# Optimization experiments

Hardware: AMD Instinct MI355X
Metric: run time of the kernel (lower is better)

Reference implementation:

```python
import jax, jax.numpy as jnp
import numpy as np


def setup_inputs() -> dict:
    key = jax.random.key(0)
    k1, k2, k3, k4, k5 = jax.random.split(key, 5)
    b, c, l, h, w = 16, 64, 8, 56, 56
    cl = c * l
    return {
        "inpt": jax.random.normal(k1, (b, c, l, h, w), dtype=jnp.float32),
        "theta_w": jax.random.normal(k2, (cl,), dtype=jnp.float32) * (1.0 / np.sqrt(cl)),
        "g_w": jax.random.normal(k3, (cl,), dtype=jnp.float32) * (1.0 / np.sqrt(cl)),
        "h_w": jax.random.normal(k4, (cl,), dtype=jnp.float32),
        "h_b": jax.random.normal(k5, (cl,), dtype=jnp.float32) * 0.1,
    }


def reference(inpt, theta_w, g_w, h_w, h_b):
    # inpt: [b, c, l, h, w] -> flatten channel/time to cl and space to n = h*w
    b, c, l, h, w = inpt.shape
    cl, n = c * l, h * w
    x = inpt.reshape(b, cl, n)  # [b, cl, n]

    # 1x1 convs (bias=False) projecting cl -> 1 channel
    t = jnp.einsum("bcn,c->bn", x, theta_w)  # theta(inpt): [b, n]
    g = jnp.einsum("bcn,c->bn", x, g_w)      # g(inpt):     [b, n]

    # torch: outer product t (b,1,n) * g^T (b,n,1) -> [b,n,n], AvgPool1d(n) over last dim
    # mathematically: att[b,i] = g[b,i] * mean_j t[b,j]
    att = g * jnp.mean(t, axis=1, keepdims=True)  # [b, n]

    # h: 1x1 conv 1 -> cl channels with bias, then residual add
    out = x + att[:, None, :] * h_w[None, :, None] + h_b[None, :, None]  # [b, cl, n]
    return out.reshape(b, cl, h, w)
```

## Files before the change

kernel.cpp:

```cpp
#include <hip/hip_runtime.h>

#define BATCH 16
#define CL    512
#define NSP   3136
#define N4    (NSP / 4)
#define CGROUPS 4
#define CPG   (CL / CGROUPS)

__global__ __launch_bounds__(256) void sa_pass1(
    const float* __restrict__ x,
    const float* __restrict__ theta_w,
    const float* __restrict__ g_w,
    float* __restrict__ g_out,
    float* __restrict__ m_out)
{
    const int b     = blockIdx.x;
    const int chunk = blockIdx.y;
    const int tid   = threadIdx.x;
    const int tx    = tid & 63;
    const int ty    = tid >> 6;
    const int i4    = chunk * 64 + tx;
    const bool valid = (i4 < N4);

    const float4* xb = (const float4*)(x + (size_t)b * CL * NSP);

    float4 gv = make_float4(0.f, 0.f, 0.f, 0.f);
    float4 tv = make_float4(0.f, 0.f, 0.f, 0.f);
    if (valid) {
        const int c0 = ty * CPG;
        #pragma unroll 4
        for (int c = c0; c < c0 + CPG; ++c) {
            float4 xv = xb[(size_t)c * N4 + i4];
            float gw = g_w[c];
            float tw = theta_w[c];
            gv.x += xv.x * gw; gv.y += xv.y * gw;
            gv.z += xv.z * gw; gv.w += xv.w * gw;
            tv.x += xv.x * tw; tv.y += xv.y * tw;
            tv.z += xv.z * tw; tv.w += xv.w * tw;
        }
    }

    __shared__ float4 sg[CGROUPS][64];
    __shared__ float4 st[CGROUPS][64];
    sg[ty][tx] = gv;
    st[ty][tx] = tv;
    __syncthreads();

    if (ty == 0) {
        float4 G = sg[0][tx];
        float4 T = st[0][tx];
        #pragma unroll
        for (int k = 1; k < CGROUPS; ++k) {
            float4 a = sg[k][tx];
            float4 t2 = st[k][tx];
            G.x += a.x;  G.y += a.y;  G.z += a.z;  G.w += a.w;
            T.x += t2.x; T.y += t2.y; T.z += t2.z; T.w += t2.w;
        }
        if (valid)
            ((float4*)g_out)[(size_t)b * N4 + i4] = G;

        float s = T.x + T.y + T.z + T.w;
        #pragma unroll
        for (int off = 32; off > 0; off >>= 1)
            s += __shfl_down(s, off, 64);
        if (tx == 0)
            atomicAdd(&m_out[b], s);
    }
}

__global__ __launch_bounds__(256) void sa_pass2(
    const float* __restrict__ x,
    const float* __restrict__ g_arr,
    const float* __restrict__ m_arr,
    const float* __restrict__ h_w,
    const float* __restrict__ h_b,
    float* __restrict__ out)
{
    const int f = blockIdx.x * blockDim.x + threadIdx.x;
    const int total4 = BATCH * CL * N4;
    if (f >= total4) return;

    const int i4 = f % N4;
    const int bc = f / N4;
    const int c  = bc & (CL - 1);
    const int b  = bc >> 9;

    float4 xv = ((const float4*)x)[f];
    float4 gv = ((const float4*)g_arr)[(size_t)b * N4 + i4];
    float  m  = m_arr[b] * (1.0f / (float)NSP);
    float  hw = h_w[c];
    float  hb = h_b[c];

    float4 o;
    o.x = xv.x + m * gv.x * hw + hb;
    o.y = xv.y + m * gv.y * hw + hb;
    o.z = xv.z + m * gv.z * hw + hb;
    o.w = xv.w + m * gv.w * hw + hb;
    ((float4*)out)[f] = o;
}

extern "C" void kernel_launch(void* const* d_in, const int* in_sizes, int n_in,
                              void* d_out, int out_size, void* d_ws, size_t ws_size,
                              hipStream_t stream)
{
    const float* x       = (const float*)d_in[0];
    const float* theta_w = (const float*)d_in[1];
    const float* g_w     = (const float*)d_in[2];
    const float* h_w     = (const float*)d_in[3];
    const float* h_b     = (const float*)d_in[4];
    float* out = (float*)d_out;

    float* m_ws = (float*)d_ws;
    float* g_ws = (float*)((char*)d_ws + 256);

    hipMemsetAsync(m_ws, 0, BATCH * sizeof(float), stream);

    dim3 grid1(BATCH, (N4 + 63) / 64);
    sa_pass1<<<grid1, 256, 0, stream>>>(x, theta_w, g_w, g_ws, m_ws);

    const int total4 = BATCH * CL * N4;
    sa_pass2<<<(total4 + 255) / 256, 256, 0, stream>>>(x, g_ws, m_ws, h_w, h_b, out);
}
```

Before: 203.0 us.

## Split reduction finer, replace atomics with partial sums, nontemporal stores

```diff
diff --git a/kernel.cpp b/kernel.cpp
--- a/kernel.cpp
+++ b/kernel.cpp
@@ -4,30 +4,34 @@
 #define CL    512
 #define NSP   3136
 #define N4    (NSP / 4)
-#define CGROUPS 4
-#define CPG   (CL / CGROUPS)
+#define CHUNK 32
+#define NCHUNK ((N4 + CHUNK - 1) / CHUNK)
+#define GROUPS 8
+#define CPG   (CL / GROUPS)
+
+typedef float nfloat4 __attribute__((ext_vector_type(4)));
 
 __global__ __launch_bounds__(256) void sa_pass1(
     const float* __restrict__ x,
     const float* __restrict__ theta_w,
     const float* __restrict__ g_w,
     float* __restrict__ g_out,
-    float* __restrict__ m_out)
+    float* __restrict__ t_part)
 {
     const int b     = blockIdx.x;
     const int chunk = blockIdx.y;
     const int tid   = threadIdx.x;
-    const int tx    = tid & 63;
-    const int ty    = tid >> 6;
-    const int i4    = chunk * 64 + tx;
+    const int tx    = tid & 31;
+    const int gq    = tid >> 5;
+    const int i4    = chunk * CHUNK + tx;
     const bool valid = (i4 < N4);
 
-    const float4* xb = (const float4*)(x + (size_t)b * CL * NSP);
+    const float4* xb = (const float4*)x + (size_t)b * CL * N4;
 
     float4 gv = make_float4(0.f, 0.f, 0.f, 0.f);
     float4 tv = make_float4(0.f, 0.f, 0.f, 0.f);
     if (valid) {
-        const int c0 = ty * CPG;
+        const int c0 = gq * CPG;
         #pragma unroll 4
         for (int c = c0; c < c0 + CPG; ++c) {
             float4 xv = xb[(size_t)c * N4 + i4];
@@ -40,18 +44,18 @@
         }
     }
 
-    __shared__ float4 sg[CGROUPS][64];
-    __shared__ float4 st[CGROUPS][64];
-    sg[ty][tx] = gv;
-    st[ty][tx] = tv;
+    __shared__ float4 sg[GROUPS][CHUNK];
+    __shared__ float4 st[GROUPS][CHUNK];
+    sg[gq][tx] = gv;
+    st[gq][tx] = tv;
     __syncthreads();
 
-    if (ty == 0) {
+    if (tid < 32) {
         float4 G = sg[0][tx];
         float4 T = st[0][tx];
         #pragma unroll
-        for (int k = 1; k < CGROUPS; ++k) {
-            float4 a = sg[k][tx];
+        for (int k = 1; k < GROUPS; ++k) {
+            float4 a  = sg[k][tx];
             float4 t2 = st[k][tx];
             G.x += a.x;  G.y += a.y;  G.z += a.z;  G.w += a.w;
             T.x += t2.x; T.y += t2.y; T.z += t2.z; T.w += t2.w;
@@ -61,42 +65,58 @@
 
         float s = T.x + T.y + T.z + T.w;
         #pragma unroll
-        for (int off = 32; off > 0; off >>= 1)
-            s += __shfl_down(s, off, 64);
+        for (int off = 16; off > 0; off >>= 1)
+            s += __shfl_down(s, off, 32);
         if (tx == 0)
-            atomicAdd(&m_out[b], s);
+            t_part[b * NCHUNK + chunk] = s;
     }
 }
 
+#define P2_F4_PER_BLOCK 512
 __global__ __launch_bounds__(256) void sa_pass2(
     const float* __restrict__ x,
     const float* __restrict__ g_arr,
-    const float* __restrict__ m_arr,
+    const float* __restrict__ t_part,
     const float* __restrict__ h_w,
     const float* __restrict__ h_b,
     float* __restrict__ out)
 {
-    const int f = blockIdx.x * blockDim.x + threadIdx.x;
-    const int total4 = BATCH * CL * N4;
-    if (f >= total4) return;
+    const int blk = blockIdx.x;
+    const int b   = blk / ((CL * N4) / P2_F4_PER_BLOCK);
 
-    const int i4 = f % N4;
-    const int bc = f / N4;
-    const int c  = bc & (CL - 1);
-    const int b  = bc >> 9;
+    __shared__ float sm;
+    if (threadIdx.x < 32) {
+        float v = (threadIdx.x < NCHUNK) ? t_part[b * NCHUNK + threadIdx.x] : 0.f;
+        #pragma unroll
+        for (int off = 16; off > 0; off >>= 1)
+            v += __shfl_down(v, off, 32);
+        if (threadIdx.x == 0)
+            sm = v * (1.0f / (float)NSP);
+    }
+    __syncthreads();
+    const float m = sm;
 
-    float4 xv = ((const float4*)x)[f];
-    float4 gv = ((const float4*)g_arr)[(size_t)b * N4 + i4];
-    float  m  = m_arr[b] * (1.0f / (float)NSP);
-    float  hw = h_w[c];
-    float  hb = h_b[c];
+    const size_t base = (size_t)blk * P2_F4_PER_BLOCK + threadIdx.x;
+    #pragma unroll
+    for (int r = 0; r < P2_F4_PER_BLOCK / 256; ++r) {
+        const size_t f = base + (size_t)r * 256;
+        const int i4 = (int)(f % N4);
+        const int bc = (int)(f / N4);
+        const int c  = bc & (CL - 1);
 
-    float4 o;
-    o.x = xv.x + m * gv.x * hw + hb;
-    o.y = xv.y + m * gv.y * hw + hb;
-    o.z = xv.z + m * gv.z * hw + hb;
-    o.w = xv.w + m * gv.w * hw + hb;
-    ((float4*)out)[f] = o;
+        float4 xv = ((const float4*)x)[f];
+        float4 gv = ((const float4*)g_arr)[(size_t)b * N4 + i4];
+        const float hw = h_w[c];
+        const float hb = h_b[c];
+        const float mh = m * hw;
+
+        nfloat4 o;
+        o.x = xv.x + mh * gv.x + hb;
+        o.y = xv.y + mh * gv.y + hb;
+        o.z = xv.z + mh * gv.z + hb;
+        o.w = xv.w + mh * gv.w + hb;
+        __builtin_nontemporal_store(o, (nfloat4*)out + f);
+    }
 }
 
 extern "C" void kernel_launch(void* const* d_in, const int* in_sizes, int n_in,
@@ -110,14 +130,12 @@
     const float* h_b     = (const float*)d_in[4];
     float* out = (float*)d_out;
 
-    float* m_ws = (float*)d_ws;
-    float* g_ws = (float*)((char*)d_ws + 256);
+    float* t_ws = (float*)d_ws;
+    float* g_ws = (float*)((char*)d_ws + 2048);
 
-    hipMemsetAsync(m_ws, 0, BATCH * sizeof(float), stream);
-
-    dim3 grid1(BATCH, (N4 + 63) / 64);
-    sa_pass1<<<grid1, 256, 0, stream>>>(x, theta_w, g_w, g_ws, m_ws);
+    dim3 grid1(BATCH, NCHUNK);
+    sa_pass1<<<grid1, 256, 0, stream>>>(x, theta_w, g_w, g_ws, t_ws);
 
     const int total4 = BATCH * CL * N4;
-    sa_pass2<<<(total4 + 255) / 256, 256, 0, stream>>>(x, g_ws, m_ws, h_w, h_b, out);
+    sa_pass2<<<total4 / P2_F4_PER_BLOCK, 256, 0, stream>>>(x, g_ws, t_ws, h_w, h_b, out);
 }
```

Result: no change. 200.4 us (-1.3%).
